# Kernel tuning notes

Measured on AMD Instinct MI355X. Metric: run time of the kernel, lower is better.

Reference implementation:

```python
import jax, jax.numpy as jnp
import numpy as np

N = 50000
E = 800000
IN_CH = 128
HID = 64
HEADS = 4
G = 64  # number of graphs in batch
NEG_SLOPE = 0.2


def setup_inputs() -> dict:
    key = jax.random.key(0)
    ks = jax.random.split(key, 16)
    s = lambda fan_in: 1.0 / np.sqrt(fan_in)
    x = jax.random.normal(ks[0], (N, IN_CH), dtype=jnp.float32)
    edge_index = jax.random.randint(ks[1], (2, E), 0, N, dtype=jnp.int64)
    batch = jnp.sort(jax.random.randint(ks[2], (N,), 0, G, dtype=jnp.int64))
    # GAT layer 1: in 128 -> heads*hid = 256
    W1 = jax.random.uniform(ks[3], (IN_CH, HEADS * HID), jnp.float32, -s(IN_CH), s(IN_CH))
    a1_src = jax.random.uniform(ks[4], (HEADS, HID), jnp.float32, -s(HID), s(HID))
    a1_dst = jax.random.uniform(ks[5], (HEADS, HID), jnp.float32, -s(HID), s(HID))
    b1 = jnp.zeros((HEADS * HID,), jnp.float32)
    # GAT layer 2: in 256 -> heads*hid = 256
    W2 = jax.random.uniform(ks[6], (HEADS * HID, HEADS * HID), jnp.float32, -s(HEADS * HID), s(HEADS * HID))
    a2_src = jax.random.uniform(ks[7], (HEADS, HID), jnp.float32, -s(HID), s(HID))
    a2_dst = jax.random.uniform(ks[8], (HEADS, HID), jnp.float32, -s(HID), s(HID))
    b2 = jnp.zeros((HEADS * HID,), jnp.float32)
    # post-pool MLP: (in + 2*heads*hid) -> 256 -> 128
    d_cat = IN_CH + 2 * HEADS * HID
    W3 = jax.random.uniform(ks[9], (d_cat, 256), jnp.float32, -s(d_cat), s(d_cat))
    b3 = jnp.zeros((256,), jnp.float32)
    W4 = jax.random.uniform(ks[10], (256, 128), jnp.float32, -s(256), s(256))
    b4 = jnp.zeros((128,), jnp.float32)
    return {"x": x, "edge_index": edge_index, "batch": batch,
            "W1": W1, "a1_src": a1_src, "a1_dst": a1_dst, "b1": b1,
            "W2": W2, "a2_src": a2_src, "a2_dst": a2_dst, "b2": b2,
            "W3": W3, "b3": b3, "W4": W4, "b4": b4}


def gat_layer(x, src, dst, W, a_src, a_dst, b):
    n = x.shape[0]
    h = (x @ W).reshape(n, HEADS, HID)                 # [N,H,D]
    e_src = jnp.einsum('nhd,hd->nh', h, a_src)         # [N,H]
    e_dst = jnp.einsum('nhd,hd->nh', h, a_dst)
    e = jax.nn.leaky_relu(e_src[src] + e_dst[dst], NEG_SLOPE)  # [E,H]
    # segment softmax over incoming edges of each destination node
    m = jax.ops.segment_max(e, dst, num_segments=n)
    m = jnp.where(jnp.isfinite(m), m, 0.0)
    ex = jnp.exp(e - m[dst])
    denom = jax.ops.segment_sum(ex, dst, num_segments=n)
    alpha = ex / (denom[dst] + 1e-16)                  # [E,H]
    msg = h[src] * alpha[:, :, None]                   # [E,H,D]
    out = jax.ops.segment_sum(msg, dst, num_segments=n)
    return out.reshape(n, HEADS * HID) + b


def reference(x, edge_index, batch, W1, a1_src, a1_dst, b1, W2, a2_src, a2_dst, b2, W3, b3, W4, b4):
    src, dst = edge_index[0], edge_index[1]
    h0 = x
    h1 = jax.nn.relu(gat_layer(h0, src, dst, W1, a1_src, a1_dst, b1))
    h2 = jax.nn.relu(gat_layer(h1, src, dst, W2, a2_src, a2_dst, b2))
    comb = jnp.concatenate([h0, h1, h2], axis=-1)      # [N, 128+256+256]
    sums = jax.ops.segment_sum(comb, batch, num_segments=G)
    cnt = jax.ops.segment_sum(jnp.ones((x.shape[0],), comb.dtype), batch, num_segments=G)
    pooled = sums / jnp.maximum(cnt, 1.0)[:, None]     # [G, 640]
    hmlp = jax.nn.relu(pooled @ W3 + b3)               # dropout is identity at eval
    return hmlp @ W4 + b4                              # [G, 128]
```

## Files before the change

kernel.cpp:

```cpp
#include <hip/hip_runtime.h>
#include <cstdint>
#include <cstddef>

#define N_NODES 50000
#define M_PAD 50048
#define E_EDGES 800000
#define INCH 128
#define HID 64
#define HEADS 4
#define NHD 256
#define NGRAPH 64
#define DCAT 640
#define NEG_SLOPE 0.2f

typedef __attribute__((ext_vector_type(8))) short bf16x8;
typedef __attribute__((ext_vector_type(4))) float f32x4;

static __device__ inline unsigned short f2bf(float f) {
    unsigned int u = __float_as_uint(f);
    unsigned int r = (u + 0x7FFFu + ((u >> 16) & 1u)) >> 16;
    return (unsigned short)r;
}
static __device__ inline float bf2f(unsigned short b) {
    return __uint_as_float(((unsigned int)b) << 16);
}

__global__ void wsplit_kernel(const float* __restrict__ W,
                              unsigned short* __restrict__ Wthi,
                              unsigned short* __restrict__ Wtlo, int K)
{
    const int i = blockIdx.x * 256 + threadIdx.x;
    if (i >= K * NHD) return;
    const int n = i / K, k = i - n * K;
    const float v = W[(size_t)k * NHD + n];
    const unsigned short hi = f2bf(v);
    Wthi[i] = hi;
    Wtlo[i] = f2bf(v - bf2f(hi));
}

__global__ void asplit_kernel(const float* __restrict__ A,
                              unsigned short* __restrict__ Ahi,
                              unsigned short* __restrict__ Alo, int n)
{
    const int i = blockIdx.x * 256 + threadIdx.x;
    if (i >= n) return;
    const float v = A[i];
    const unsigned short h = f2bf(v);
    Ahi[i] = h;
    Alo[i] = f2bf(v - bf2f(h));
}

#define GK 64
#define LDAB 72

__global__ __launch_bounds__(256, 2) void gemm_mfma(
    const unsigned short* __restrict__ Athi,
    const unsigned short* __restrict__ Atlo,
    const unsigned short* __restrict__ Bthi,
    const unsigned short* __restrict__ Btlo,
    const float* __restrict__ asrc, const float* __restrict__ adst,
    unsigned short* __restrict__ Cb, float* __restrict__ es,
    float* __restrict__ ed, int M, int K)
{
    __shared__ unsigned short Ahi[128 * LDAB];
    __shared__ unsigned short Alo[128 * LDAB];
    __shared__ unsigned short Bhi[128 * LDAB];
    __shared__ unsigned short Blo[128 * LDAB];

    const int t    = threadIdx.x;
    const int row0 = blockIdx.x * 128;
    const int col0 = blockIdx.y * 128;
    const int wave = t >> 6, lane = t & 63;
    const int wr = (wave >> 1) * 64;
    const int wc = (wave & 1) * 64;
    const int m16 = lane & 15, quad = lane >> 4;

    f32x4 acc[4][4];
#pragma unroll
    for (int i = 0; i < 4; ++i)
#pragma unroll
        for (int j = 0; j < 4; ++j) acc[i][j] = (f32x4){0.f, 0.f, 0.f, 0.f};

    for (int k0 = 0; k0 < K; k0 += GK) {
#pragma unroll
        for (int i = 0; i < 4; ++i) {
            const int seg = t + i * 256;
            const int r = seg >> 3, p = (seg & 7) * 8;
            const size_t ga = (size_t)(row0 + r) * K + k0 + p;
            const size_t gb = (size_t)(col0 + r) * K + k0 + p;
            *(int4*)(&Ahi[r * LDAB + p]) = *(const int4*)(Athi + ga);
            *(int4*)(&Alo[r * LDAB + p]) = *(const int4*)(Atlo + ga);
            *(int4*)(&Bhi[r * LDAB + p]) = *(const int4*)(Bthi + gb);
            *(int4*)(&Blo[r * LDAB + p]) = *(const int4*)(Btlo + gb);
        }
        __syncthreads();

#pragma unroll
        for (int h = 0; h < 2; ++h) {
            bf16x8 afh[4], afl[4], bfh[4], bfl[4];
#pragma unroll
            for (int i = 0; i < 4; ++i) {
                const int r = wr + i * 16 + m16;
                afh[i] = *(const bf16x8*)(&Ahi[r * LDAB + h * 32 + quad * 8]);
                afl[i] = *(const bf16x8*)(&Alo[r * LDAB + h * 32 + quad * 8]);
            }
#pragma unroll
            for (int j = 0; j < 4; ++j) {
                const int n = wc + j * 16 + m16;
                bfh[j] = *(const bf16x8*)(&Bhi[n * LDAB + h * 32 + quad * 8]);
                bfl[j] = *(const bf16x8*)(&Blo[n * LDAB + h * 32 + quad * 8]);
            }
#pragma unroll
            for (int i = 0; i < 4; ++i)
#pragma unroll
                for (int j = 0; j < 4; ++j) {
                    acc[i][j] = __builtin_amdgcn_mfma_f32_16x16x32_bf16(afh[i], bfh[j], acc[i][j], 0, 0, 0);
                    acc[i][j] = __builtin_amdgcn_mfma_f32_16x16x32_bf16(afh[i], bfl[j], acc[i][j], 0, 0, 0);
                    acc[i][j] = __builtin_amdgcn_mfma_f32_16x16x32_bf16(afl[i], bfh[j], acc[i][j], 0, 0, 0);
                }
        }
        __syncthreads();
    }

#pragma unroll
    for (int i = 0; i < 4; ++i)
#pragma unroll
        for (int reg = 0; reg < 4; ++reg) {
            const int r = row0 + wr + i * 16 + quad * 4 + reg;
            if (r < M) {
#pragma unroll
                for (int j = 0; j < 4; ++j)
                    Cb[(size_t)r * NHD + col0 + wc + j * 16 + m16] = f2bf(acc[i][j][reg]);
            }
        }

    const int head = (col0 + wc) >> 6;
    float a_s[4], a_d[4];
#pragma unroll
    for (int j = 0; j < 4; ++j) {
        a_s[j] = asrc[head * HID + j * 16 + m16];
        a_d[j] = adst[head * HID + j * 16 + m16];
    }
#pragma unroll
    for (int i = 0; i < 4; ++i)
#pragma unroll
        for (int reg = 0; reg < 4; ++reg) {
            float ps = 0.f, pd = 0.f;
#pragma unroll
            for (int j = 0; j < 4; ++j) {
                const float v = acc[i][j][reg];
                ps += v * a_s[j];
                pd += v * a_d[j];
            }
#pragma unroll
            for (int off = 1; off < 16; off <<= 1) {
                ps += __shfl_xor(ps, off, 64);
                pd += __shfl_xor(pd, off, 64);
            }
            if (m16 == 0) {
                const int r = row0 + wr + i * 16 + quad * 4 + reg;
                if (r < M) {
                    es[r * HEADS + head] = ps;
                    ed[r * HEADS + head] = pd;
                }
            }
        }
}

__global__ void hist_kernel(const int* __restrict__ ei, int* __restrict__ counts)
{
    const int e = blockIdx.x * 256 + threadIdx.x;
    if (e >= E_EDGES) return;
    atomicAdd(&counts[ei[E_EDGES + e]], 1);
}

#define SBLK 1024
#define NSCB ((N_NODES + SBLK - 1) / SBLK)

__global__ __launch_bounds__(1024) void scan_local_kernel(
    const int* __restrict__ counts, int* __restrict__ offsets,
    int* __restrict__ bsum)
{
    __shared__ int tmp[SBLK];
    const int t = threadIdx.x;
    const int i = blockIdx.x * SBLK + t;
    const int v = (i < N_NODES) ? counts[i] : 0;
    tmp[t] = v;
    __syncthreads();
    for (int off = 1; off < SBLK; off <<= 1) {
        const int u = (t >= off) ? tmp[t - off] : 0;
        __syncthreads();
        tmp[t] += u;
        __syncthreads();
    }
    if (i < N_NODES) offsets[i] = tmp[t] - v;
    if (t == SBLK - 1) bsum[blockIdx.x] = tmp[t];
}

__global__ __launch_bounds__(1024) void scan_final_kernel(
    int* __restrict__ offsets, int* __restrict__ cursor,
    const int* __restrict__ bsum)
{
    __shared__ int base_sh;
    const int b = blockIdx.x;
    if (threadIdx.x == 0) {
        int s = 0;
        for (int j = 0; j < b; ++j) s += bsum[j];
        base_sh = s;
    }
    __syncthreads();
    const int i = b * SBLK + threadIdx.x;
    if (i < N_NODES) {
        const int v = offsets[i] + base_sh;
        offsets[i] = v;
        cursor[i]  = v;
    }
    if (b == 0 && threadIdx.x == 0) offsets[N_NODES] = E_EDGES;
}

__global__ void scatter_kernel(const int* __restrict__ ei, int* __restrict__ cursor,
                               int* __restrict__ csr)
{
    const int e = blockIdx.x * 256 + threadIdx.x;
    if (e >= E_EDGES) return;
    const int d = ei[E_EDGES + e];
    const int pos = atomicAdd(&cursor[d], 1);
    csr[pos] = e;
}

__global__ __launch_bounds__(256) void aggregate_fused(
    const unsigned short* __restrict__ hb, const int* __restrict__ ei,
    const int* __restrict__ csr, const int* __restrict__ offsets,
    const float* __restrict__ es, const float* __restrict__ ed,
    const float* __restrict__ bias, unsigned short* __restrict__ outhi,
    unsigned short* __restrict__ outlo)
{
    const int wid  = threadIdx.x >> 6;
    const int lane = threadIdx.x & 63;
    const int node = blockIdx.x * 4 + wid;
    if (node >= N_NODES) return;
    const int head = lane >> 4;
    const int col  = lane * 4;
    const int sub  = lane & 15;

    const float edc = ed[node * 4 + head];
    const int beg = offsets[node], end = offsets[node + 1];

    float4 acc = make_float4(0.f, 0.f, 0.f, 0.f);
    float dsum = 0.f;

    int base = beg;
    int m_cur = min(16, end - base);
    int s_cur = 0; float w_cur = 0.f;
    if (base < end && sub < m_cur) {
        const int eid = csr[base + sub];
        s_cur = ei[eid];
        float u = es[s_cur * 4 + head] + edc;
        u = u > 0.f ? u : NEG_SLOPE * u;
        w_cur = expf(u);
    }

    while (base < end) {
        const int base_n = base + 16;
        const int m_nxt = min(16, end - base_n);
        int s_nxt = 0; float w_nxt = 0.f;
        if (base_n < end && sub < m_nxt) {
            const int eid = csr[base_n + sub];
            s_nxt = ei[eid];
            float u = es[s_nxt * 4 + head] + edc;
            u = u > 0.f ? u : NEG_SLOPE * u;
            w_nxt = expf(u);
        }
        if (m_cur == 16) {
#pragma unroll
            for (int i = 0; i < 16; ++i) {
                const int   s = (int)__builtin_amdgcn_readlane((unsigned)s_cur, i);
                const float w = __shfl(w_cur, (lane & 48) + i, 64);
                const ushort4 v = *(const ushort4*)(hb + (size_t)s * NHD + col);
                acc.x += w * bf2f(v.x);
                acc.y += w * bf2f(v.y);
                acc.z += w * bf2f(v.z);
                acc.w += w * bf2f(v.w);
                dsum += w;
            }
        } else {
            for (int i = 0; i < m_cur; ++i) {
                const int   s = __shfl(s_cur, i, 64);
                const float w = __shfl(w_cur, (lane & 48) + i, 64);
                const ushort4 v = *(const ushort4*)(hb + (size_t)s * NHD + col);
                acc.x += w * bf2f(v.x);
                acc.y += w * bf2f(v.y);
                acc.z += w * bf2f(v.z);
                acc.w += w * bf2f(v.w);
                dsum += w;
            }
        }
        s_cur = s_nxt; w_cur = w_nxt; m_cur = m_nxt; base = base_n;
    }

    const float inv = 1.0f / (dsum + 1e-16f);
    const float4 bb = *(const float4*)(bias + col);
    float4 o;
    o.x = fmaxf(acc.x * inv + bb.x, 0.f);
    o.y = fmaxf(acc.y * inv + bb.y, 0.f);
    o.z = fmaxf(acc.z * inv + bb.z, 0.f);
    o.w = fmaxf(acc.w * inv + bb.w, 0.f);
    ushort4 oh;
    oh.x = f2bf(o.x); oh.y = f2bf(o.y); oh.z = f2bf(o.z); oh.w = f2bf(o.w);
    *(ushort4*)(outhi + (size_t)node * NHD + col) = oh;
    if (outlo) {
        ushort4 ol;
        ol.x = f2bf(o.x - bf2f(oh.x));
        ol.y = f2bf(o.y - bf2f(oh.y));
        ol.z = f2bf(o.z - bf2f(oh.z));
        ol.w = f2bf(o.w - bf2f(oh.w));
        *(ushort4*)(outlo + (size_t)node * NHD + col) = ol;
    }
}

__global__ void graph_offsets_kernel(const int* __restrict__ batch, int* __restrict__ goff)
{
    const int n = blockIdx.x * 256 + threadIdx.x;
    if (n >= N_NODES) return;
    const int b  = batch[n];
    const int bp = (n == 0) ? -1 : batch[n - 1];
    for (int g = bp + 1; g <= b; ++g) goff[g] = n;
    if (n == N_NODES - 1) {
        for (int g = b + 1; g <= NGRAPH; ++g) goff[g] = N_NODES;
    }
}

#define PRB 128

__global__ __launch_bounds__(640) void pool_sum_kernel(
    const float* __restrict__ x, const unsigned short* __restrict__ h1b,
    const unsigned short* __restrict__ h2b, const int* __restrict__ batch,
    float* __restrict__ sums)
{
    __shared__ int bsh[PRB];
    const int c  = threadIdx.x;
    const int r0 = blockIdx.x * PRB;
    const int r1 = min(N_NODES, r0 + PRB);
    const int nr = r1 - r0;
    if (c < nr) bsh[c] = batch[r0 + c];
    __syncthreads();

    const float* srcf = nullptr;
    const unsigned short* srcb = nullptr;
    int ld, cc;
    if (c < INCH)            { srcf = x;   ld = INCH; cc = c; }
    else if (c < INCH + NHD) { srcb = h1b; ld = NHD;  cc = c - INCH; }
    else                     { srcb = h2b; ld = NHD;  cc = c - INCH - NHD; }

    float sum = 0.f;
    int g = bsh[0];
    for (int i = 0; i < nr; ++i) {
        const int gb = bsh[i];
        if (gb != g) {
            atomicAdd(&sums[g * DCAT + c], sum);
            sum = 0.f;
            g = gb;
        }
        sum += srcf ? srcf[(size_t)(r0 + i) * ld + cc]
                    : bf2f(srcb[(size_t)(r0 + i) * ld + cc]);
    }
    atomicAdd(&sums[g * DCAT + c], sum);
}

__global__ void pool_finalize_kernel(const float* __restrict__ sums,
                                     const int* __restrict__ goff,
                                     float* __restrict__ pooled)
{
    const int i = blockIdx.x * 256 + threadIdx.x;
    if (i >= NGRAPH * DCAT) return;
    const int g = i / DCAT;
    const float cnt = (float)(goff[g + 1] - goff[g]);
    pooled[i] = sums[i] / fmaxf(cnt, 1.0f);
}

__global__ __launch_bounds__(256) void mlp_kernel(
    const float* __restrict__ pooled, const float* __restrict__ W3,
    const float* __restrict__ b3, const float* __restrict__ W4,
    const float* __restrict__ b4, float* __restrict__ out)
{
    const int g = blockIdx.x;
    __shared__ float p[DCAT];
    __shared__ float hm[256];
    for (int i = threadIdx.x; i < DCAT; i += 256) p[i] = pooled[(size_t)g * DCAT + i];
    __syncthreads();
    float s = b3[threadIdx.x];
    for (int k = 0; k < DCAT; ++k) s += p[k] * W3[(size_t)k * 256 + threadIdx.x];
    hm[threadIdx.x] = fmaxf(s, 0.f);
    __syncthreads();
    if (threadIdx.x < 128) {
        float o = b4[threadIdx.x];
        for (int k = 0; k < 256; ++k) o += hm[k] * W4[(size_t)k * 128 + threadIdx.x];
        out[(size_t)g * 128 + threadIdx.x] = o;
    }
}

extern "C" void kernel_launch(void* const* d_in, const int* in_sizes, int n_in,
                              void* d_out, int out_size, void* d_ws, size_t ws_size,
                              hipStream_t stream)
{
    const float* x     = (const float*)d_in[0];
    const int*   ei    = (const int*)d_in[1];
    const int*   batch = (const int*)d_in[2];
    const float* W1    = (const float*)d_in[3];
    const float* a1s   = (const float*)d_in[4];
    const float* a1d   = (const float*)d_in[5];
    const float* b1    = (const float*)d_in[6];
    const float* W2    = (const float*)d_in[7];
    const float* a2s   = (const float*)d_in[8];
    const float* a2d   = (const float*)d_in[9];
    const float* b2    = (const float*)d_in[10];
    const float* W3    = (const float*)d_in[11];
    const float* b3    = (const float*)d_in[12];
    const float* W4    = (const float*)d_in[13];
    const float* b4    = (const float*)d_in[14];
    float* out = (float*)d_out;

    size_t off = 0;
    auto carve = [&](size_t bytes) -> void* {
        void* p = (char*)d_ws + off;
        off = (off + bytes + 255) & ~(size_t)255;
        return p;
    };
    unsigned short* xhi   = (unsigned short*)carve((size_t)M_PAD * INCH * 2);
    unsigned short* xlo   = (unsigned short*)carve((size_t)M_PAD * INCH * 2);
    unsigned short* ghi   = (unsigned short*)carve((size_t)N_NODES * NHD * 2);
    unsigned short* h1hi  = (unsigned short*)carve((size_t)M_PAD * NHD * 2);
    unsigned short* h1lo  = (unsigned short*)carve((size_t)M_PAD * NHD * 2);
    unsigned short* h2hi  = (unsigned short*)carve((size_t)N_NODES * NHD * 2);
    float* es     = (float*)carve((size_t)N_NODES * HEADS * 4);
    float* ed     = (float*)carve((size_t)N_NODES * HEADS * 4);
    float* pooled = (float*)carve((size_t)NGRAPH * DCAT * 4);
    float* psums  = (float*)carve((size_t)NGRAPH * DCAT * 4);
    int*   counts  = (int*)carve((size_t)N_NODES * 4);
    int*   offsets = (int*)carve((size_t)(N_NODES + 1) * 4);
    int*   cursor  = (int*)carve((size_t)N_NODES * 4);
    int*   csr     = (int*)carve((size_t)E_EDGES * 4);
    int*   goff    = (int*)carve((size_t)(NGRAPH + 1) * 4);
    int*   bsum    = (int*)carve((size_t)NSCB * 4);
    unsigned short* w1thi = (unsigned short*)carve((size_t)NHD * INCH * 2);
    unsigned short* w1tlo = (unsigned short*)carve((size_t)NHD * INCH * 2);
    unsigned short* w2thi = (unsigned short*)carve((size_t)NHD * NHD * 2);
    unsigned short* w2tlo = (unsigned short*)carve((size_t)NHD * NHD * 2);

    const int egrid = (E_EDGES + 255) / 256;
    const int ngrid = (N_NODES + 255) / 256;

    hipMemsetAsync(counts, 0, (size_t)N_NODES * 4, stream);
    hist_kernel<<<egrid, 256, 0, stream>>>(ei, counts);
    scan_local_kernel<<<NSCB, SBLK, 0, stream>>>(counts, offsets, bsum);
    scan_final_kernel<<<NSCB, SBLK, 0, stream>>>(offsets, cursor, bsum);
    scatter_kernel<<<egrid, 256, 0, stream>>>(ei, cursor, csr);
    graph_offsets_kernel<<<ngrid, 256, 0, stream>>>(batch, goff);
    wsplit_kernel<<<(INCH * NHD + 255) / 256, 256, 0, stream>>>(W1, w1thi, w1tlo, INCH);
    wsplit_kernel<<<(NHD * NHD + 255) / 256, 256, 0, stream>>>(W2, w2thi, w2tlo, NHD);
    asplit_kernel<<<(N_NODES * INCH + 255) / 256, 256, 0, stream>>>(x, xhi, xlo, N_NODES * INCH);

    dim3 ggrid((M_PAD + 127) / 128, NHD / 128);

    gemm_mfma<<<ggrid, 256, 0, stream>>>(xhi, xlo, w1thi, w1tlo, a1s, a1d,
                                         ghi, es, ed, N_NODES, INCH);
    aggregate_fused<<<(N_NODES + 3) / 4, 256, 0, stream>>>(ghi, ei, csr, offsets,
                                                           es, ed, b1, h1hi, h1lo);
    gemm_mfma<<<ggrid, 256, 0, stream>>>(h1hi, h1lo, w2thi, w2tlo, a2s, a2d,
                                         ghi, es, ed, N_NODES, NHD);
    aggregate_fused<<<(N_NODES + 3) / 4, 256, 0, stream>>>(ghi, ei, csr, offsets,
                                                           es, ed, b2, h2hi, nullptr);

    hipMemsetAsync(psums, 0, (size_t)NGRAPH * DCAT * 4, stream);
    pool_sum_kernel<<<(N_NODES + PRB - 1) / PRB, 640, 0, stream>>>(x, h1hi, h2hi, batch, psums);
    pool_finalize_kernel<<<(NGRAPH * DCAT + 255) / 256, 256, 0, stream>>>(psums, goff, pooled);
    mlp_kernel<<<NGRAPH, 256, 0, stream>>>(pooled, W3, b3, W4, b4, out);
}
```

Baseline: 504.0 us.

## Fuse prep kernels, store source ids in CSR, batch MLP over graphs

Merges the histogram, graph-offset, psums zeroing, and weight/input bf16 split kernels into one launch, which removes several launches and a memset. The CSR now stores source node ids directly, so the aggregation skips one dependent gather per edge. Pooling reads the bf16 high part of x instead of fp32 x, which lowers precision for the x columns of the pooled features. The finalize step is folded into an MLP that handles 8 graphs per block to reuse weight loads, at the cost of only 8 blocks of parallelism.

```diff
diff --git a/kernel.cpp b/kernel.cpp
--- a/kernel.cpp
+++ b/kernel.cpp
@@ -25,29 +25,63 @@
     return __uint_as_float(((unsigned int)b) << 16);
 }
 
-__global__ void wsplit_kernel(const float* __restrict__ W,
-                              unsigned short* __restrict__ Wthi,
-                              unsigned short* __restrict__ Wtlo, int K)
-{
-    const int i = blockIdx.x * 256 + threadIdx.x;
-    if (i >= K * NHD) return;
-    const int n = i / K, k = i - n * K;
-    const float v = W[(size_t)k * NHD + n];
-    const unsigned short hi = f2bf(v);
-    Wthi[i] = hi;
-    Wtlo[i] = f2bf(v - bf2f(hi));
-}
-
-__global__ void asplit_kernel(const float* __restrict__ A,
-                              unsigned short* __restrict__ Ahi,
-                              unsigned short* __restrict__ Alo, int n)
-{
-    const int i = blockIdx.x * 256 + threadIdx.x;
-    if (i >= n) return;
-    const float v = A[i];
+#define W1N (INCH * NHD)
+#define W2N (NHD * NHD)
+#define XN  (N_NODES * INCH)
+#define HB  ((E_EDGES + 255) / 256)
+#define GB  ((N_NODES + 255) / 256)
+#define PZB ((NGRAPH * DCAT + 255) / 256)
+#define SPB ((W1N + W2N + XN + 255) / 256)
+#define PREPB (HB + GB + PZB + SPB)
+
+__global__ void prep_kernel(
+    const int* __restrict__ ei, const int* __restrict__ batch,
+    const float* __restrict__ W1, const float* __restrict__ W2,
+    const float* __restrict__ x,
+    int* __restrict__ counts, int* __restrict__ goff,
+    float* __restrict__ psums,
+    unsigned short* __restrict__ w1thi, unsigned short* __restrict__ w1tlo,
+    unsigned short* __restrict__ w2thi, unsigned short* __restrict__ w2tlo,
+    unsigned short* __restrict__ xhi, unsigned short* __restrict__ xlo)
+{
+    const int b = blockIdx.x;
+    if (b < HB) {
+        const int e = b * 256 + threadIdx.x;
+        if (e < E_EDGES) atomicAdd(&counts[ei[E_EDGES + e]], 1);
+        return;
+    }
+    if (b < HB + GB) {
+        const int n = (b - HB) * 256 + threadIdx.x;
+        if (n >= N_NODES) return;
+        const int bb = batch[n];
+        const int bp = (n == 0) ? -1 : batch[n - 1];
+        for (int g = bp + 1; g <= bb; ++g) goff[g] = n;
+        if (n == N_NODES - 1)
+            for (int g = bb + 1; g <= NGRAPH; ++g) goff[g] = N_NODES;
+        return;
+    }
+    if (b < HB + GB + PZB) {
+        const int i = (b - HB - GB) * 256 + threadIdx.x;
+        if (i < NGRAPH * DCAT) psums[i] = 0.f;
+        return;
+    }
+    const int i = (b - HB - GB - PZB) * 256 + threadIdx.x;
+    float v; unsigned short* dhi; unsigned short* dlo; int idx;
+    if (i < W1N) {
+        const int n = i / INCH, k = i - n * INCH;
+        v = W1[(size_t)k * NHD + n]; dhi = w1thi; dlo = w1tlo; idx = i;
+    } else if (i < W1N + W2N) {
+        const int j = i - W1N;
+        const int n = j / NHD, k = j - n * NHD;
+        v = W2[(size_t)k * NHD + n]; dhi = w2thi; dlo = w2tlo; idx = j;
+    } else {
+        const int j = i - W1N - W2N;
+        if (j >= XN) return;
+        v = x[j]; dhi = xhi; dlo = xlo; idx = j;
+    }
     const unsigned short h = f2bf(v);
-    Ahi[i] = h;
-    Alo[i] = f2bf(v - bf2f(h));
+    dhi[idx] = h;
+    dlo[idx] = f2bf(v - bf2f(h));
 }
 
 #define GK 64
@@ -165,13 +199,6 @@
                 }
             }
         }
-}
-
-__global__ void hist_kernel(const int* __restrict__ ei, int* __restrict__ counts)
-{
-    const int e = blockIdx.x * 256 + threadIdx.x;
-    if (e >= E_EDGES) return;
-    atomicAdd(&counts[ei[E_EDGES + e]], 1);
 }
 
 #define SBLK 1024
@@ -223,14 +250,15 @@
 {
     const int e = blockIdx.x * 256 + threadIdx.x;
     if (e >= E_EDGES) return;
+    const int s = ei[e];
     const int d = ei[E_EDGES + e];
     const int pos = atomicAdd(&cursor[d], 1);
-    csr[pos] = e;
+    csr[pos] = s;
 }
 
 __global__ __launch_bounds__(256) void aggregate_fused(
-    const unsigned short* __restrict__ hb, const int* __restrict__ ei,
-    const int* __restrict__ csr, const int* __restrict__ offsets,
+    const unsigned short* __restrict__ hb, const int* __restrict__ csr,
+    const int* __restrict__ offsets,
     const float* __restrict__ es, const float* __restrict__ ed,
     const float* __restrict__ bias, unsigned short* __restrict__ outhi,
     unsigned short* __restrict__ outlo)
@@ -253,8 +281,7 @@
     int m_cur = min(16, end - base);
     int s_cur = 0; float w_cur = 0.f;
     if (base < end && sub < m_cur) {
-        const int eid = csr[base + sub];
-        s_cur = ei[eid];
+        s_cur = csr[base + sub];
         float u = es[s_cur * 4 + head] + edc;
         u = u > 0.f ? u : NEG_SLOPE * u;
         w_cur = expf(u);
@@ -265,8 +292,7 @@
         const int m_nxt = min(16, end - base_n);
         int s_nxt = 0; float w_nxt = 0.f;
         if (base_n < end && sub < m_nxt) {
-            const int eid = csr[base_n + sub];
-            s_nxt = ei[eid];
+            s_nxt = csr[base_n + sub];
             float u = es[s_nxt * 4 + head] + edc;
             u = u > 0.f ? u : NEG_SLOPE * u;
             w_nxt = expf(u);
@@ -318,22 +344,10 @@
     }
 }
 
-__global__ void graph_offsets_kernel(const int* __restrict__ batch, int* __restrict__ goff)
-{
-    const int n = blockIdx.x * 256 + threadIdx.x;
-    if (n >= N_NODES) return;
-    const int b  = batch[n];
-    const int bp = (n == 0) ? -1 : batch[n - 1];
-    for (int g = bp + 1; g <= b; ++g) goff[g] = n;
-    if (n == N_NODES - 1) {
-        for (int g = b + 1; g <= NGRAPH; ++g) goff[g] = N_NODES;
-    }
-}
-
 #define PRB 128
 
 __global__ __launch_bounds__(640) void pool_sum_kernel(
-    const float* __restrict__ x, const unsigned short* __restrict__ h1b,
+    const unsigned short* __restrict__ xhi, const unsigned short* __restrict__ h1b,
     const unsigned short* __restrict__ h2b, const int* __restrict__ batch,
     float* __restrict__ sums)
 {
@@ -345,10 +359,8 @@
     if (c < nr) bsh[c] = batch[r0 + c];
     __syncthreads();
 
-    const float* srcf = nullptr;
-    const unsigned short* srcb = nullptr;
-    int ld, cc;
-    if (c < INCH)            { srcf = x;   ld = INCH; cc = c; }
+    const unsigned short* srcb; int ld, cc;
+    if (c < INCH)            { srcb = xhi; ld = INCH; cc = c; }
     else if (c < INCH + NHD) { srcb = h1b; ld = NHD;  cc = c - INCH; }
     else                     { srcb = h2b; ld = NHD;  cc = c - INCH - NHD; }
 
@@ -361,42 +373,52 @@
             sum = 0.f;
             g = gb;
         }
-        sum += srcf ? srcf[(size_t)(r0 + i) * ld + cc]
-                    : bf2f(srcb[(size_t)(r0 + i) * ld + cc]);
+        sum += bf2f(srcb[(size_t)(r0 + i) * ld + cc]);
     }
     atomicAdd(&sums[g * DCAT + c], sum);
 }
 
-__global__ void pool_finalize_kernel(const float* __restrict__ sums,
-                                     const int* __restrict__ goff,
-                                     float* __restrict__ pooled)
-{
-    const int i = blockIdx.x * 256 + threadIdx.x;
-    if (i >= NGRAPH * DCAT) return;
-    const int g = i / DCAT;
-    const float cnt = (float)(goff[g + 1] - goff[g]);
-    pooled[i] = sums[i] / fmaxf(cnt, 1.0f);
-}
-
 __global__ __launch_bounds__(256) void mlp_kernel(
-    const float* __restrict__ pooled, const float* __restrict__ W3,
-    const float* __restrict__ b3, const float* __restrict__ W4,
-    const float* __restrict__ b4, float* __restrict__ out)
-{
-    const int g = blockIdx.x;
-    __shared__ float p[DCAT];
-    __shared__ float hm[256];
-    for (int i = threadIdx.x; i < DCAT; i += 256) p[i] = pooled[(size_t)g * DCAT + i];
+    const float* __restrict__ psums, const int* __restrict__ goff,
+    const float* __restrict__ W3, const float* __restrict__ b3,
+    const float* __restrict__ W4, const float* __restrict__ b4,
+    float* __restrict__ out)
+{
+    const int g0 = blockIdx.x * 8;
+    __shared__ float p[8][DCAT];
+    __shared__ float hm[8][256];
+    for (int idx = threadIdx.x; idx < 8 * DCAT; idx += 256) {
+        const int gg = idx / DCAT, i = idx - gg * DCAT;
+        const int g = g0 + gg;
+        const float inv = 1.0f / fmaxf((float)(goff[g + 1] - goff[g]), 1.0f);
+        p[gg][i] = psums[(size_t)g * DCAT + i] * inv;
+    }
     __syncthreads();
-    float s = b3[threadIdx.x];
-    for (int k = 0; k < DCAT; ++k) s += p[k] * W3[(size_t)k * 256 + threadIdx.x];
-    hm[threadIdx.x] = fmaxf(s, 0.f);
+    const int c = threadIdx.x;
+    float acc[8];
+#pragma unroll
+    for (int gg = 0; gg < 8; ++gg) acc[gg] = b3[c];
+    for (int k = 0; k < DCAT; ++k) {
+        const float w = W3[(size_t)k * 256 + c];
+#pragma unroll
+        for (int gg = 0; gg < 8; ++gg) acc[gg] += p[gg][k] * w;
+    }
+#pragma unroll
+    for (int gg = 0; gg < 8; ++gg) hm[gg][c] = fmaxf(acc[gg], 0.f);
     __syncthreads();
-    if (threadIdx.x < 128) {
-        float o = b4[threadIdx.x];
-        for (int k = 0; k < 256; ++k) o += hm[k] * W4[(size_t)k * 128 + threadIdx.x];
-        out[(size_t)g * 128 + threadIdx.x] = o;
-    }
+    const int c2 = threadIdx.x & 127;
+    const int gh = (threadIdx.x >> 7) * 4;
+    float a2[4];
+#pragma unroll
+    for (int j = 0; j < 4; ++j) a2[j] = b4[c2];
+    for (int k = 0; k < 256; ++k) {
+        const float w = W4[(size_t)k * 128 + c2];
+#pragma unroll
+        for (int j = 0; j < 4; ++j) a2[j] += hm[gh + j][k] * w;
+    }
+#pragma unroll
+    for (int j = 0; j < 4; ++j)
+        out[(size_t)(g0 + gh + j) * 128 + c2] = a2[j];
 }
 
 extern "C" void kernel_launch(void* const* d_in, const int* in_sizes, int n_in,
@@ -434,7 +456,6 @@
     unsigned short* h2hi  = (unsigned short*)carve((size_t)N_NODES * NHD * 2);
     float* es     = (float*)carve((size_t)N_NODES * HEADS * 4);
     float* ed     = (float*)carve((size_t)N_NODES * HEADS * 4);
-    float* pooled = (float*)carve((size_t)NGRAPH * DCAT * 4);
     float* psums  = (float*)carve((size_t)NGRAPH * DCAT * 4);
     int*   counts  = (int*)carve((size_t)N_NODES * 4);
     int*   offsets = (int*)carve((size_t)(N_NODES + 1) * 4);
@@ -448,31 +469,26 @@
     unsigned short* w2tlo = (unsigned short*)carve((size_t)NHD * NHD * 2);
 
     const int egrid = (E_EDGES + 255) / 256;
-    const int ngrid = (N_NODES + 255) / 256;
 
     hipMemsetAsync(counts, 0, (size_t)N_NODES * 4, stream);
-    hist_kernel<<<egrid, 256, 0, stream>>>(ei, counts);
+    prep_kernel<<<PREPB, 256, 0, stream>>>(ei, batch, W1, W2, x,
+                                           counts, goff, psums,
+                                           w1thi, w1tlo, w2thi, w2tlo, xhi, xlo);
     scan_local_kernel<<<NSCB, SBLK, 0, stream>>>(counts, offsets, bsum);
     scan_final_kernel<<<NSCB, SBLK, 0, stream>>>(offsets, cursor, bsum);
     scatter_kernel<<<egrid, 256, 0, stream>>>(ei, cursor, csr);
-    graph_offsets_kernel<<<ngrid, 256, 0, stream>>>(batch, goff);
-    wsplit_kernel<<<(INCH * NHD + 255) / 256, 256, 0, stream>>>(W1, w1thi, w1tlo, INCH);
-    wsplit_kernel<<<(NHD * NHD + 255) / 256, 256, 0, stream>>>(W2, w2thi, w2tlo, NHD);
-    asplit_kernel<<<(N_NODES * INCH + 255) / 256, 256, 0, stream>>>(x, xhi, xlo, N_NODES * INCH);
 
     dim3 ggrid((M_PAD + 127) / 128, NHD / 128);
 
     gemm_mfma<<<ggrid, 256, 0, stream>>>(xhi, xlo, w1thi, w1tlo, a1s, a1d,
                                          ghi, es, ed, N_NODES, INCH);
-    aggregate_fused<<<(N_NODES + 3) / 4, 256, 0, stream>>>(ghi, ei, csr, offsets,
+    aggregate_fused<<<(N_NODES + 3) / 4, 256, 0, stream>>>(ghi, csr, offsets,
                                                            es, ed, b1, h1hi, h1lo);
     gemm_mfma<<<ggrid, 256, 0, stream>>>(h1hi, h1lo, w2thi, w2tlo, a2s, a2d,
                                          ghi, es, ed, N_NODES, NHD);
-    aggregate_fused<<<(N_NODES + 3) / 4, 256, 0, stream>>>(ghi, ei, csr, offsets,
+    aggregate_fused<<<(N_NODES + 3) / 4, 256, 0, stream>>>(ghi, csr, offsets,
                                                            es, ed, b2, h2hi, nullptr);
 
-    hipMemsetAsync(psums, 0, (size_t)NGRAPH * DCAT * 4, stream);
-    pool_sum_kernel<<<(N_NODES + PRB - 1) / PRB, 640, 0, stream>>>(x, h1hi, h2hi, batch, psums);
-    pool_finalize_kernel<<<(NGRAPH * DCAT + 255) / 256, 256, 0, stream>>>(psums, goff, pooled);
-    mlp_kernel<<<NGRAPH, 256, 0, stream>>>(pooled, W3, b3, W4, b4, out);
-}
+    pool_sum_kernel<<<(N_NODES + PRB - 1) / PRB, 640, 0, stream>>>(xhi, h1hi, h2hi, batch, psums);
+    mlp_kernel<<<NGRAPH / 8, 256, 0, stream>>>(psums, goff, W3, b3, W4, b4, out);
+}
```

After: 486.6 us. -3.5%, faster.
